# Optimization experiments

Measured on AMD Instinct MI355X. Metric: run time of the kernel, lower is better.

## Reference

```python
import jax, jax.numpy as jnp
import numpy as np

B, T, V, E, U = 8192, 1, 4000, 256, 256
IN = E + E  # GRU input dim: concat(features[B,1,256], embedded tokens[B,1,256]) -> 512


def setup_inputs() -> dict:
    key = jax.random.key(0)
    ks = jax.random.split(key, 8)
    s = 0.05
    return {
        "tokens": jax.random.randint(ks[0], (B, T), 0, V),
        "features": jax.random.normal(ks[1], (B, E), jnp.float32),
        "hidden": jnp.zeros((B, U), jnp.float32),  # unused by the original call (gru gets no initial_state)
        "emb": jax.random.normal(ks[2], (V, E), jnp.float32) * s,
        "gru_kernel": jax.random.normal(ks[3], (IN, 3 * U), jnp.float32) * s,
        "gru_rkernel": jax.random.normal(ks[4], (U, 3 * U), jnp.float32) * s,
        "gru_bias": jnp.zeros((2, 3 * U), jnp.float32),  # reset_after=True: separate input/recurrent biases
        "fc1_w": jax.random.normal(ks[5], (U, U), jnp.float32) * s,
        "fc1_b": jnp.zeros((U,), jnp.float32),
        "fc2_w": jax.random.normal(ks[6], (U, V), jnp.float32) * s,
        "fc2_b": jnp.zeros((V,), jnp.float32),
    }


def reference(tokens, features, hidden, emb, gru_kernel, gru_rkernel, gru_bias,
              fc1_w, fc1_b, fc2_w, fc2_b):
    # Embedding lookup: [B,T,E]
    x = emb[tokens]
    # concat context vector on feature axis (forces T==1): [B,1,E+E]
    x = jnp.concatenate([features[:, None, :], x], axis=-1)
    # Keras GRU called without initial_state -> zeros initial state.
    h0 = jnp.zeros((x.shape[0], U), x.dtype)

    def step(h, xt):  # xt: [B, IN]; Keras GRU v3 (reset_after=True) cell; dropout off at inference
        gx = xt @ gru_kernel + gru_bias[0]      # [B, 3U]
        gh = h @ gru_rkernel + gru_bias[1]      # [B, 3U]
        xz, xr, xn = jnp.split(gx, 3, axis=-1)
        hz, hr, hn = jnp.split(gh, 3, axis=-1)
        z = jax.nn.sigmoid(xz + hz)
        r = jax.nn.sigmoid(xr + hr)
        n = jnp.tanh(xn + r * hn)
        h_new = z * h + (1.0 - z) * n
        return h_new, h_new

    state, seq = jax.lax.scan(step, h0, jnp.swapaxes(x, 0, 1))  # seq: [T,B,U]
    out = jnp.swapaxes(seq, 0, 1)               # [B,T,U]
    y = out @ fc1_w + fc1_b                     # [B,T,U]
    y = y.reshape(-1, y.shape[-1])              # [B*T, U]
    logits = y @ fc2_w + fc2_b                  # [B*T, V]
    return (logits, state)
```

## Files before the change

### kernel.cpp

```cpp
#include <hip/hip_runtime.h>
#include <stdint.h>

typedef unsigned short u16;
typedef __attribute__((ext_vector_type(8))) short bf16x8;
typedef __attribute__((ext_vector_type(4))) float f32x4;

#define Bsz   8192
#define Vv    4000
#define Vpad  4096
#define Ee    256
#define Uu    256
#define INd   512
#define G3    768

__device__ __forceinline__ u16 f2bf(float f) {
    union { float f; uint32_t i; } v; v.f = f;
    uint32_t x = v.i;
    return (u16)((x + 0x7fffu + ((x >> 16) & 1u)) >> 16);
}

__device__ __forceinline__ void gload16(const u16* g, u16* l) {
    __builtin_amdgcn_global_load_lds(
        (const __attribute__((address_space(1))) unsigned int*)g,
        (__attribute__((address_space(3))) unsigned int*)l, 16, 0, 0);
}

__global__ __launch_bounds__(256) void gather_x(
    const int* __restrict__ tokens, const float* __restrict__ features,
    const float* __restrict__ emb, u16* __restrict__ x)
{
    int id = blockIdx.x * 256 + threadIdx.x;
    int b = id >> 6;
    int k = (id & 63) * 8;
    const float* src = (k < Ee) ? (features + (size_t)b * Ee + k)
                                : (emb + (size_t)tokens[b] * Ee + (k - Ee));
    float4 a = *(const float4*)src;
    float4 c = *(const float4*)(src + 4);
    u16 o[8] = {f2bf(a.x), f2bf(a.y), f2bf(a.z), f2bf(a.w),
                f2bf(c.x), f2bf(c.y), f2bf(c.z), f2bf(c.w)};
    *(uint4*)(x + (size_t)b * INd + k) = *(uint4*)o;
}

__global__ __launch_bounds__(256) void transpose_all(
    const float* __restrict__ w1,  u16* __restrict__ w1t,
    const float* __restrict__ fc1, u16* __restrict__ fc1t,
    const float* __restrict__ fc2, u16* __restrict__ fc2t)
{
    __shared__ float t[32][33];
    int b = blockIdx.x;
    const float* in; u16* out; int K, N, bx, by;
    if (b < 384)      { in = w1;  out = w1t;  K = 512; N = 768;  bx = b % 24;  by = b / 24; }
    else if (b < 448) { b -= 384; in = fc1; out = fc1t; K = 256; N = 256;  bx = b % 8;   by = b / 8; }
    else              { b -= 448; in = fc2; out = fc2t; K = 256; N = Vv;   bx = b % 128; by = b / 128; }
    int n0 = bx * 32, k0 = by * 32;
    int c = threadIdx.x & 31, r = threadIdx.x >> 5;
    int n = n0 + c;
    #pragma unroll
    for (int i = 0; i < 32; i += 8)
        t[r + i][c] = (n < N) ? in[(size_t)(k0 + r + i) * N + n] : 0.f;
    __syncthreads();
    #pragma unroll
    for (int i = 0; i < 32; i += 8)
        out[(size_t)(n0 + r + i) * K + k0 + c] = f2bf(t[c][r + i]);
}

template<bool OUT_BF16>
__global__ __launch_bounds__(256) void gemm128(
    const u16* __restrict__ A, const u16* __restrict__ BT,
    const float* __restrict__ bias, void* __restrict__ Cout,
    int N, int K)
{
    __shared__ __align__(16) u16 As[128 * 32];
    __shared__ __align__(16) u16 Bs[128 * 32];

    int tid  = threadIdx.x;
    int m0   = blockIdx.y * 128;
    int n0   = blockIdx.x * 128;
    int wid  = tid >> 6;
    int lane = tid & 63;
    int quad = lane >> 4;
    int l16  = lane & 15;
    int wm   = (wid >> 1) * 64;
    int wn   = (wid & 1) * 64;

    f32x4 acc[4][4] = {};

    const u16* ag = A  + (size_t)(m0 + (tid >> 2)) * K + (tid & 3) * 8;
    const u16* bg = BT + (size_t)(n0 + (tid >> 2)) * K + (tid & 3) * 8;
    u16* lA = &As[tid * 8];
    u16* lB = &Bs[tid * 8];

    for (int k0 = 0; k0 < K; k0 += 32) {
        __syncthreads();
        gload16(ag + k0,            lA);
        gload16(ag + 64 * K + k0,   lA + 64 * 32);
        gload16(bg + k0,            lB);
        gload16(bg + 64 * K + k0,   lB + 64 * 32);
        __syncthreads();

        bf16x8 af[4], bf[4];
        #pragma unroll
        for (int i = 0; i < 4; i++)
            af[i] = *(const bf16x8*)&As[(wm + i * 16 + l16) * 32 + quad * 8];
        #pragma unroll
        for (int j = 0; j < 4; j++)
            bf[j] = *(const bf16x8*)&Bs[(wn + j * 16 + l16) * 32 + quad * 8];
        #pragma unroll
        for (int i = 0; i < 4; i++)
            #pragma unroll
            for (int j = 0; j < 4; j++)
                acc[i][j] = __builtin_amdgcn_mfma_f32_16x16x32_bf16(af[i], bf[j], acc[i][j], 0, 0, 0);
    }

    #pragma unroll
    for (int i = 0; i < 4; i++)
    #pragma unroll
    for (int j = 0; j < 4; j++) {
        int gn = n0 + wn + j * 16 + l16;
        if (gn >= N) continue;
        float bvv = bias[gn];
        #pragma unroll
        for (int r = 0; r < 4; r++) {
            int gm = m0 + wm + i * 16 + quad * 4 + r;
            float v = acc[i][j][r] + bvv;
            if (OUT_BF16) ((u16*)Cout)[(size_t)gm * N + gn] = f2bf(v);
            else          ((float*)Cout)[(size_t)gm * N + gn] = v;
        }
    }
}

__global__ __launch_bounds__(256) void gemm_gru(
    const u16* __restrict__ A,
    const u16* __restrict__ BT,
    const float* __restrict__ gb,
    u16* __restrict__ h,
    float* __restrict__ state)
{
    __shared__ __align__(16) u16 As[128 * 32];
    __shared__ __align__(16) u16 Bs[3][64 * 32];

    int tid  = threadIdx.x;
    int m0   = blockIdx.y * 128;
    int n0   = blockIdx.x * 64;
    int wid  = tid >> 6;
    int lane = tid & 63;
    int quad = lane >> 4;
    int l16  = lane & 15;
    int wm   = wid * 32;

    f32x4 acc[3][2][4] = {};

    const u16* ag = A  + (size_t)(m0 + (tid >> 2)) * INd + (tid & 3) * 8;
    const u16* bg = BT + (size_t)(n0 + (tid >> 2)) * INd + (tid & 3) * 8;
    u16* lA = &As[tid * 8];
    u16* lB = &Bs[0][tid * 8];

    for (int k0 = 0; k0 < INd; k0 += 32) {
        __syncthreads();
        gload16(ag + k0,           lA);
        gload16(ag + 64 * INd + k0, lA + 64 * 32);
        #pragma unroll
        for (int g = 0; g < 3; g++)
            gload16(bg + (size_t)g * 256 * INd + k0, lB + g * 64 * 32);
        __syncthreads();

        bf16x8 af[2];
        #pragma unroll
        for (int i = 0; i < 2; i++)
            af[i] = *(const bf16x8*)&As[(wm + i * 16 + l16) * 32 + quad * 8];
        #pragma unroll
        for (int g = 0; g < 3; g++)
            #pragma unroll
            for (int j = 0; j < 4; j++) {
                bf16x8 bf = *(const bf16x8*)&Bs[g][(j * 16 + l16) * 32 + quad * 8];
                acc[g][0][j] = __builtin_amdgcn_mfma_f32_16x16x32_bf16(af[0], bf, acc[g][0][j], 0, 0, 0);
                acc[g][1][j] = __builtin_amdgcn_mfma_f32_16x16x32_bf16(af[1], bf, acc[g][1][j], 0, 0, 0);
            }
    }

    #pragma unroll
    for (int i = 0; i < 2; i++)
    #pragma unroll
    for (int j = 0; j < 4; j++) {
        int jj = n0 + j * 16 + l16;
        float bz  = gb[jj]          + gb[G3 + jj];
        float br  = gb[Uu + jj]     + gb[G3 + Uu + jj];
        float b0n = gb[2 * Uu + jj];
        float b1n = gb[G3 + 2 * Uu + jj];
        #pragma unroll
        for (int r = 0; r < 4; r++) {
            int b = m0 + wm + i * 16 + quad * 4 + r;
            float z  = 1.f / (1.f + __expf(-(acc[0][i][j][r] + bz)));
            float rr = 1.f / (1.f + __expf(-(acc[1][i][j][r] + br)));
            float n  = tanhf(acc[2][i][j][r] + b0n + rr * b1n);
            float hv = (1.f - z) * n;
            h[(size_t)b * Uu + jj] = f2bf(hv);
            state[(size_t)b * Uu + jj] = hv;
        }
    }
}

extern "C" void kernel_launch(void* const* d_in, const int* in_sizes, int n_in,
                              void* d_out, int out_size, void* d_ws, size_t ws_size,
                              hipStream_t stream)
{
    const int*   tokens   = (const int*)d_in[0];
    const float* features = (const float*)d_in[1];
    const float* emb      = (const float*)d_in[3];
    const float* w1       = (const float*)d_in[4];
    const float* gbias    = (const float*)d_in[6];
    const float* fc1w     = (const float*)d_in[7];
    const float* fc1b     = (const float*)d_in[8];
    const float* fc2w     = (const float*)d_in[9];
    const float* fc2b     = (const float*)d_in[10];

    float* logits = (float*)d_out;
    float* state  = logits + (size_t)Bsz * Vv;

    char* ws = (char*)d_ws;
    u16* x    = (u16*)(ws);
    u16* w1t  = (u16*)(ws +  8388608);
    u16* fc1t = (u16*)(ws +  9175040);
    u16* fc2t = (u16*)(ws +  9306112);
    u16* h    = (u16*)(ws + 11403264);
    u16* y    = (u16*)(ws + 15597568);

    gather_x<<<dim3(Bsz * 64 / 256), 256, 0, stream>>>(tokens, features, emb, x);
    transpose_all<<<dim3(1472), 256, 0, stream>>>(w1, w1t, fc1w, fc1t, fc2w, fc2t);

    gemm_gru<<<dim3(Uu / 64, Bsz / 128), 256, 0, stream>>>(x, w1t, gbias, h, state);

    gemm128<true><<<dim3(Uu / 128, Bsz / 128), 256, 0, stream>>>(
        h, fc1t, fc1b, (void*)y, Uu, Uu);

    gemm128<false><<<dim3(Vpad / 128, Bsz / 128), 256, 0, stream>>>(
        y, fc2t, fc2b, (void*)logits, Vv, Uu);
}
```

Baseline: 232.1 us.

## Fuse embedding gather into GRU GEMM and shrink tiles for small GEMMs

Drops the separate gather kernel. The GRU GEMM now loads features and embedding rows directly, converts them to bf16 and writes them into shared memory, which removes the round trip of the x buffer through global memory and one launch. GRU and fc1 tiles shrink to 64 rows, giving more blocks for better CU occupancy on the smaller GEMMs, at the cost of reading weight tiles more often. The A loads in the GRU kernel are now synchronous register loads instead of async LDS loads, which may expose their latency.

Result: faster. 221.3 us (-4.7%).

```diff
diff --git a/kernel.cpp b/kernel.cpp
--- a/kernel.cpp
+++ b/kernel.cpp
@@ -23,22 +23,6 @@
     __builtin_amdgcn_global_load_lds(
         (const __attribute__((address_space(1))) unsigned int*)g,
         (__attribute__((address_space(3))) unsigned int*)l, 16, 0, 0);
-}
-
-__global__ __launch_bounds__(256) void gather_x(
-    const int* __restrict__ tokens, const float* __restrict__ features,
-    const float* __restrict__ emb, u16* __restrict__ x)
-{
-    int id = blockIdx.x * 256 + threadIdx.x;
-    int b = id >> 6;
-    int k = (id & 63) * 8;
-    const float* src = (k < Ee) ? (features + (size_t)b * Ee + k)
-                                : (emb + (size_t)tokens[b] * Ee + (k - Ee));
-    float4 a = *(const float4*)src;
-    float4 c = *(const float4*)(src + 4);
-    u16 o[8] = {f2bf(a.x), f2bf(a.y), f2bf(a.z), f2bf(a.w),
-                f2bf(c.x), f2bf(c.y), f2bf(c.z), f2bf(c.w)};
-    *(uint4*)(x + (size_t)b * INd + k) = *(uint4*)o;
 }
 
 __global__ __launch_bounds__(256) void transpose_all(
@@ -64,122 +48,57 @@
         out[(size_t)(n0 + r + i) * K + k0 + c] = f2bf(t[c][r + i]);
 }
 
-template<bool OUT_BF16>
-__global__ __launch_bounds__(256) void gemm128(
-    const u16* __restrict__ A, const u16* __restrict__ BT,
-    const float* __restrict__ bias, void* __restrict__ Cout,
-    int N, int K)
-{
-    __shared__ __align__(16) u16 As[128 * 32];
-    __shared__ __align__(16) u16 Bs[128 * 32];
-
-    int tid  = threadIdx.x;
-    int m0   = blockIdx.y * 128;
-    int n0   = blockIdx.x * 128;
-    int wid  = tid >> 6;
-    int lane = tid & 63;
-    int quad = lane >> 4;
-    int l16  = lane & 15;
-    int wm   = (wid >> 1) * 64;
-    int wn   = (wid & 1) * 64;
-
-    f32x4 acc[4][4] = {};
-
-    const u16* ag = A  + (size_t)(m0 + (tid >> 2)) * K + (tid & 3) * 8;
-    const u16* bg = BT + (size_t)(n0 + (tid >> 2)) * K + (tid & 3) * 8;
-    u16* lA = &As[tid * 8];
-    u16* lB = &Bs[tid * 8];
-
-    for (int k0 = 0; k0 < K; k0 += 32) {
-        __syncthreads();
-        gload16(ag + k0,            lA);
-        gload16(ag + 64 * K + k0,   lA + 64 * 32);
-        gload16(bg + k0,            lB);
-        gload16(bg + 64 * K + k0,   lB + 64 * 32);
-        __syncthreads();
-
-        bf16x8 af[4], bf[4];
-        #pragma unroll
-        for (int i = 0; i < 4; i++)
-            af[i] = *(const bf16x8*)&As[(wm + i * 16 + l16) * 32 + quad * 8];
-        #pragma unroll
-        for (int j = 0; j < 4; j++)
-            bf[j] = *(const bf16x8*)&Bs[(wn + j * 16 + l16) * 32 + quad * 8];
-        #pragma unroll
-        for (int i = 0; i < 4; i++)
-            #pragma unroll
-            for (int j = 0; j < 4; j++)
-                acc[i][j] = __builtin_amdgcn_mfma_f32_16x16x32_bf16(af[i], bf[j], acc[i][j], 0, 0, 0);
-    }
-
-    #pragma unroll
-    for (int i = 0; i < 4; i++)
-    #pragma unroll
-    for (int j = 0; j < 4; j++) {
-        int gn = n0 + wn + j * 16 + l16;
-        if (gn >= N) continue;
-        float bvv = bias[gn];
-        #pragma unroll
-        for (int r = 0; r < 4; r++) {
-            int gm = m0 + wm + i * 16 + quad * 4 + r;
-            float v = acc[i][j][r] + bvv;
-            if (OUT_BF16) ((u16*)Cout)[(size_t)gm * N + gn] = f2bf(v);
-            else          ((float*)Cout)[(size_t)gm * N + gn] = v;
-        }
-    }
-}
-
-__global__ __launch_bounds__(256) void gemm_gru(
-    const u16* __restrict__ A,
-    const u16* __restrict__ BT,
+__global__ __launch_bounds__(256) void gru_fused(
+    const int* __restrict__ tokens, const float* __restrict__ features,
+    const float* __restrict__ emb,  const u16* __restrict__ BT,
     const float* __restrict__ gb,
     u16* __restrict__ h,
     float* __restrict__ state)
 {
-    __shared__ __align__(16) u16 As[128 * 32];
+    __shared__ __align__(16) u16 As[64 * 32];
     __shared__ __align__(16) u16 Bs[3][64 * 32];
-
-    int tid  = threadIdx.x;
-    int m0   = blockIdx.y * 128;
-    int n0   = blockIdx.x * 64;
-    int wid  = tid >> 6;
-    int lane = tid & 63;
-    int quad = lane >> 4;
-    int l16  = lane & 15;
-    int wm   = wid * 32;
-
-    f32x4 acc[3][2][4] = {};
-
-    const u16* ag = A  + (size_t)(m0 + (tid >> 2)) * INd + (tid & 3) * 8;
-    const u16* bg = BT + (size_t)(n0 + (tid >> 2)) * INd + (tid & 3) * 8;
-    u16* lA = &As[tid * 8];
+    __shared__ int tok[64];
+
+    int tid = threadIdx.x;
+    int m0  = blockIdx.y * 64;
+    int n0  = blockIdx.x * 64;
+    if (tid < 64) tok[tid] = tokens[m0 + tid];
+
+    int wid = tid >> 6, lane = tid & 63, quad = lane >> 4, l16 = lane & 15;
+    int wm = wid * 16;
+
+    f32x4 acc[3][4] = {};
+
+    int r  = tid >> 2;
+    int kc = (tid & 3) * 8;
+    const u16* bg = BT + (size_t)(n0 + r) * INd + kc;
     u16* lB = &Bs[0][tid * 8];
+    const float* fsrc = features + (size_t)(m0 + r) * Ee + kc;
 
     for (int k0 = 0; k0 < INd; k0 += 32) {
         __syncthreads();
-        gload16(ag + k0,           lA);
-        gload16(ag + 64 * INd + k0, lA + 64 * 32);
         #pragma unroll
         for (int g = 0; g < 3; g++)
             gload16(bg + (size_t)g * 256 * INd + k0, lB + g * 64 * 32);
-        __syncthreads();
-
-        bf16x8 af[2];
-        #pragma unroll
-        for (int i = 0; i < 2; i++)
-            af[i] = *(const bf16x8*)&As[(wm + i * 16 + l16) * 32 + quad * 8];
+        const float* src = (k0 < Ee) ? (fsrc + k0)
+                                     : (emb + (size_t)tok[r] * Ee + (k0 - Ee) + kc);
+        float4 a = *(const float4*)src;
+        float4 c = *(const float4*)(src + 4);
+        u16 o[8] = {f2bf(a.x), f2bf(a.y), f2bf(a.z), f2bf(a.w),
+                    f2bf(c.x), f2bf(c.y), f2bf(c.z), f2bf(c.w)};
+        *(uint4*)&As[tid * 8] = *(uint4*)o;
+        __syncthreads();
+
+        bf16x8 af = *(const bf16x8*)&As[(wm + l16) * 32 + quad * 8];
         #pragma unroll
         for (int g = 0; g < 3; g++)
             #pragma unroll
             for (int j = 0; j < 4; j++) {
                 bf16x8 bf = *(const bf16x8*)&Bs[g][(j * 16 + l16) * 32 + quad * 8];
-                acc[g][0][j] = __builtin_amdgcn_mfma_f32_16x16x32_bf16(af[0], bf, acc[g][0][j], 0, 0, 0);
-                acc[g][1][j] = __builtin_amdgcn_mfma_f32_16x16x32_bf16(af[1], bf, acc[g][1][j], 0, 0, 0);
+                acc[g][j] = __builtin_amdgcn_mfma_f32_16x16x32_bf16(af, bf, acc[g][j], 0, 0, 0);
             }
     }
 
-    #pragma unroll
-    for (int i = 0; i < 2; i++)
     #pragma unroll
     for (int j = 0; j < 4; j++) {
         int jj = n0 + j * 16 + l16;
@@ -188,14 +107,83 @@
         float b0n = gb[2 * Uu + jj];
         float b1n = gb[G3 + 2 * Uu + jj];
         #pragma unroll
-        for (int r = 0; r < 4; r++) {
-            int b = m0 + wm + i * 16 + quad * 4 + r;
-            float z  = 1.f / (1.f + __expf(-(acc[0][i][j][r] + bz)));
-            float rr = 1.f / (1.f + __expf(-(acc[1][i][j][r] + br)));
-            float n  = tanhf(acc[2][i][j][r] + b0n + rr * b1n);
+        for (int rr = 0; rr < 4; rr++) {
+            int b = m0 + wm + quad * 4 + rr;
+            float z  = 1.f / (1.f + __expf(-(acc[0][j][rr] + bz)));
+            float rg = 1.f / (1.f + __expf(-(acc[1][j][rr] + br)));
+            float n  = tanhf(acc[2][j][rr] + b0n + rg * b1n);
             float hv = (1.f - z) * n;
             h[(size_t)b * Uu + jj] = f2bf(hv);
             state[(size_t)b * Uu + jj] = hv;
+        }
+    }
+}
+
+template<int BMt, int BNt, bool OUT_BF16>
+__global__ __launch_bounds__(256) void gemm_bt(
+    const u16* __restrict__ A, const u16* __restrict__ BT,
+    const float* __restrict__ bias, void* __restrict__ Cout,
+    int N, int K)
+{
+    constexpr int NW_N  = (BNt == 128) ? 2 : 1;
+    constexpr int NW_M  = 4 / NW_N;
+    constexpr int WROWS = BMt / NW_M;
+    constexpr int MI    = WROWS / 16;
+
+    __shared__ __align__(16) u16 As[BMt * 32];
+    __shared__ __align__(16) u16 Bs[BNt * 32];
+
+    int tid  = threadIdx.x;
+    int m0   = blockIdx.y * BMt;
+    int n0   = blockIdx.x * BNt;
+    int wid  = tid >> 6, lane = tid & 63, quad = lane >> 4, l16 = lane & 15;
+    int wm   = (wid / NW_N) * WROWS;
+    int wn   = (wid % NW_N) * 64;
+
+    f32x4 acc[MI][4] = {};
+
+    const u16* ag = A  + (size_t)(m0 + (tid >> 2)) * K + (tid & 3) * 8;
+    const u16* bg = BT + (size_t)(n0 + (tid >> 2)) * K + (tid & 3) * 8;
+    u16* lA = &As[tid * 8];
+    u16* lB = &Bs[tid * 8];
+
+    for (int k0 = 0; k0 < K; k0 += 32) {
+        __syncthreads();
+        #pragma unroll
+        for (int s = 0; s < BMt / 64; s++)
+            gload16(ag + (size_t)s * 64 * K + k0, lA + s * 64 * 32);
+        #pragma unroll
+        for (int s = 0; s < BNt / 64; s++)
+            gload16(bg + (size_t)s * 64 * K + k0, lB + s * 64 * 32);
+        __syncthreads();
+
+        bf16x8 af[MI], bf[4];
+        #pragma unroll
+        for (int i = 0; i < MI; i++)
+            af[i] = *(const bf16x8*)&As[(wm + i * 16 + l16) * 32 + quad * 8];
+        #pragma unroll
+        for (int j = 0; j < 4; j++)
+            bf[j] = *(const bf16x8*)&Bs[(wn + j * 16 + l16) * 32 + quad * 8];
+        #pragma unroll
+        for (int i = 0; i < MI; i++)
+            #pragma unroll
+            for (int j = 0; j < 4; j++)
+                acc[i][j] = __builtin_amdgcn_mfma_f32_16x16x32_bf16(af[i], bf[j], acc[i][j], 0, 0, 0);
+    }
+
+    #pragma unroll
+    for (int i = 0; i < MI; i++)
+    #pragma unroll
+    for (int j = 0; j < 4; j++) {
+        int gn = n0 + wn + j * 16 + l16;
+        if (gn >= N) continue;
+        float bv = bias[gn];
+        #pragma unroll
+        for (int r = 0; r < 4; r++) {
+            int gm = m0 + wm + i * 16 + quad * 4 + r;
+            float v = acc[i][j][r] + bv;
+            if (OUT_BF16) ((u16*)Cout)[(size_t)gm * N + gn] = f2bf(v);
+            else          ((float*)Cout)[(size_t)gm * N + gn] = v;
         }
     }
 }
@@ -218,21 +206,20 @@
     float* state  = logits + (size_t)Bsz * Vv;
 
     char* ws = (char*)d_ws;
-    u16* x    = (u16*)(ws);
-    u16* w1t  = (u16*)(ws +  8388608);
-    u16* fc1t = (u16*)(ws +  9175040);
-    u16* fc2t = (u16*)(ws +  9306112);
-    u16* h    = (u16*)(ws + 11403264);
-    u16* y    = (u16*)(ws + 15597568);
-
-    gather_x<<<dim3(Bsz * 64 / 256), 256, 0, stream>>>(tokens, features, emb, x);
+    u16* w1t  = (u16*)(ws);
+    u16* fc1t = (u16*)(ws +   786432);
+    u16* fc2t = (u16*)(ws +   917504);
+    u16* h    = (u16*)(ws +  3014656);
+    u16* y    = (u16*)(ws +  7208960);
+
     transpose_all<<<dim3(1472), 256, 0, stream>>>(w1, w1t, fc1w, fc1t, fc2w, fc2t);
 
-    gemm_gru<<<dim3(Uu / 64, Bsz / 128), 256, 0, stream>>>(x, w1t, gbias, h, state);
-
-    gemm128<true><<<dim3(Uu / 128, Bsz / 128), 256, 0, stream>>>(
+    gru_fused<<<dim3(Uu / 64, Bsz / 64), 256, 0, stream>>>(
+        tokens, features, emb, w1t, gbias, h, state);
+
+    gemm_bt<64, 64, true><<<dim3(Uu / 64, Bsz / 64), 256, 0, stream>>>(
         h, fc1t, fc1b, (void*)y, Uu, Uu);
 
-    gemm128<false><<<dim3(Vpad / 128, Bsz / 128), 256, 0, stream>>>(
+    gemm_bt<128, 128, false><<<dim3(Vpad / 128, Bsz / 128), 256, 0, stream>>>(
         y, fc2t, fc2b, (void*)logits, Vv, Uu);
 }
```
